# Optimization experiments

Hardware: AMD Instinct MI355X
Metric: run time of the kernel (lower is better)

Reference implementation:

```python
import jax, jax.numpy as jnp
import numpy as np


def setup_inputs() -> dict:
    key = jax.random.key(0)
    ks = jax.random.split(key, 8)
    B, D, S, H, W = 32, 256, 64, 64, 64
    L = H * W
    return {
        "x": jax.random.normal(ks[0], (B, D, L), jnp.float32),
        "H": H,
        "W": W,
        "w_bcdt": jax.random.normal(ks[1], (3 * S, D), jnp.float32) * 0.02,
        "b_bcdt": jnp.zeros((3 * S,), jnp.float32),
        "w_dw": jax.random.normal(ks[2], (3 * S, 1, 3, 3), jnp.float32) * 0.1,
        "b_dw": jnp.zeros((3 * S,), jnp.float32),
        "w_hz": jax.random.normal(ks[3], (2 * D, D), jnp.float32) * 0.02,
        "b_hz": jnp.zeros((2 * D,), jnp.float32),
        "w_out": jax.random.normal(ks[4], (D, D), jnp.float32) * 0.02,
        "b_out": jnp.zeros((D,), jnp.float32),
        "A_param": jax.random.uniform(ks[5], (S,), jnp.float32, minval=1.0, maxval=16.0),
        "D_param": jnp.ones((1,), jnp.float32),
    }


def reference(x, H, W, w_bcdt, b_bcdt, w_dw, b_dw, w_hz, b_hz, w_out, b_out, A_param, D_param):
    batch, d_model, L = x.shape
    S = A_param.shape[0]
    # BCdt_proj: pointwise conv1d -> (B, 3S, L)
    bcdt = jnp.einsum('oc,bcl->bol', w_bcdt, x) + b_bcdt[None, :, None]
    # depthwise 3x3 conv over (H, W)
    x4 = bcdt.reshape(batch, 3 * S, H, W)
    x4 = jax.lax.conv_general_dilated(
        x4, w_dw, window_strides=(1, 1), padding=((1, 1), (1, 1)),
        dimension_numbers=('NCHW', 'OIHW', 'NCHW'), feature_group_count=3 * S,
    ) + b_dw[None, :, None, None]
    bcdt = x4.reshape(batch, 3 * S, L)
    Bm, Cm, dt = jnp.split(bcdt, 3, axis=1)  # each (B, S, L)
    # gating: softmax over sequence dim L
    Aw = jax.nn.softmax(dt + A_param[None, :, None], axis=-1)
    AB = Aw * Bm  # (B, S, L)
    # global state compression: h = x @ AB^T -> (B, d_model, S)
    h = jnp.einsum('bdl,bsl->bds', x, AB)
    # hz_proj (pointwise conv1d over length S)
    hz = jnp.einsum('oc,bcs->bos', w_hz, h) + b_hz[None, :, None]
    h2, z = jnp.split(hz, 2, axis=1)  # each (B, d_inner, S)
    g = h2 * jax.nn.silu(z) + h2 * D_param[0]
    hout = jnp.einsum('oc,bcs->bos', w_out, g) + b_out[None, :, None]  # (B, d_model, S)
    # expand back: y = h @ C -> (B, d_model, L)
    y = jnp.einsum('bds,bsl->bdl', hout, Cm).reshape(batch, d_model, H, W)
    return (y, hout)
```

## Files before the change

kernel.cpp:

```cpp
#include <hip/hip_runtime.h>
#include <math.h>

#define B_  32
#define D_  256
#define L_  4096
#define S_  64
#define C3_ 192

#define YSZ    ((size_t)B_ * D_ * L_)
#define HOUTSZ ((size_t)B_ * D_ * S_)
#define NCHUNK 8

typedef __attribute__((ext_vector_type(8))) short short8;
typedef __attribute__((ext_vector_type(4))) float f32x4;
typedef unsigned short ushort_t;
typedef unsigned int uint_t;

__device__ __forceinline__ short f2bf(float f) {
    __bf16 h = (__bf16)f;
    return __builtin_bit_cast(short, h);
}
__device__ __forceinline__ float bf2f(ushort_t u) {
    return __uint_as_float((uint_t)u << 16);
}
__device__ __forceinline__ short8 ld_cvt8(const float* p) {
    const float4* q = reinterpret_cast<const float4*>(p);
    float4 p0 = q[0], p1 = q[1];
    short8 s;
    s[0] = f2bf(p0.x); s[1] = f2bf(p0.y); s[2] = f2bf(p0.z); s[3] = f2bf(p0.w);
    s[4] = f2bf(p1.x); s[5] = f2bf(p1.y); s[6] = f2bf(p1.z); s[7] = f2bf(p1.w);
    return s;
}

__global__ __launch_bounds__(256) void k1_bcdt_mfma(
    const float* __restrict__ x, const float* __restrict__ w,
    const float* __restrict__ bias, ushort_t* __restrict__ out)
{
    __shared__ __align__(16) short A_lds[192][40];
    __shared__ __align__(16) short B_lds[128][40];
    const int l0 = blockIdx.x * 128;
    const int b  = blockIdx.y;
    const int tid  = threadIdx.x;
    const int lane = tid & 63;
    const int wv   = tid >> 6;
    const int lm   = lane & 15;
    const int kg   = lane >> 4;
    const float* xb = x + (size_t)b * D_ * L_;

    f32x4 acc[12][2];
    #pragma unroll
    for (int mi = 0; mi < 12; ++mi)
        #pragma unroll
        for (int nj = 0; nj < 2; ++nj)
            acc[mi][nj] = (f32x4){0.f, 0.f, 0.f, 0.f};

    for (int k0 = 0; k0 < D_; k0 += 32) {
        if (k0) __syncthreads();
        #pragma unroll
        for (int q = 0; q < 3; ++q) {
            int task = q * 256 + tid;
            int o = task >> 2, kk = (task & 3) * 8;
            *(short8*)&A_lds[o][kk] = ld_cvt8(w + (size_t)o * D_ + k0 + kk);
        }
        {
            int lp = tid & 63;
            int kgs = tid >> 6;
            const float* xp = xb + (size_t)(k0 + kgs * 8) * L_ + l0 + lp * 2;
            float2 v[8];
            #pragma unroll
            for (int r = 0; r < 8; ++r)
                v[r] = *reinterpret_cast<const float2*>(xp + (size_t)r * L_);
            short8 s0, s1;
            #pragma unroll
            for (int r = 0; r < 8; ++r) { s0[r] = f2bf(v[r].x); s1[r] = f2bf(v[r].y); }
            *(short8*)&B_lds[lp * 2][kgs * 8]     = s0;
            *(short8*)&B_lds[lp * 2 + 1][kgs * 8] = s1;
        }
        __syncthreads();
        short8 bb[2];
        #pragma unroll
        for (int nj = 0; nj < 2; ++nj)
            bb[nj] = *(const short8*)&B_lds[wv * 32 + nj * 16 + lm][kg * 8];
        #pragma unroll
        for (int mi = 0; mi < 12; ++mi) {
            short8 a = *(const short8*)&A_lds[mi * 16 + lm][kg * 8];
            #pragma unroll
            for (int nj = 0; nj < 2; ++nj)
                acc[mi][nj] = __builtin_amdgcn_mfma_f32_16x16x32_bf16(
                    a, bb[nj], acc[mi][nj], 0, 0, 0);
        }
    }
    ushort_t* ob = out + (size_t)b * C3_ * L_;
    const int col = l0 + wv * 32 + lm;
    #pragma unroll
    for (int mi = 0; mi < 12; ++mi) {
        #pragma unroll
        for (int r = 0; r < 4; ++r) {
            int o = mi * 16 + kg * 4 + r;
            float bv = bias[o];
            #pragma unroll
            for (int nj = 0; nj < 2; ++nj)
                ob[(size_t)o * L_ + col + nj * 16] =
                    (ushort_t)f2bf(acc[mi][nj][r] + bv);
        }
    }
}

__global__ __launch_bounds__(256) void k2_conv(
    const ushort_t* __restrict__ pre, const float* __restrict__ wdw,
    const float* __restrict__ bdw, ushort_t* __restrict__ cm,
    ushort_t* __restrict__ ab)
{
    __shared__ float sm[66][66];
    __shared__ float red[4];
    const int t   = blockIdx.x;
    const int b   = blockIdx.y;
    const int s   = t & 63;
    const int tid = threadIdx.x;

    for (int i = tid; i < 66 * 66; i += 256) (&sm[0][0])[i] = 0.f;
    __syncthreads();

    if (t < 64) {
        const int c = 64 + s;
        const uint_t* ip32 = reinterpret_cast<const uint_t*>(
            pre + ((size_t)b * C3_ + c) * L_);
        for (int p2 = tid; p2 < 2048; p2 += 256) {
            uint_t v = ip32[p2];
            int q = p2 * 2;
            sm[(q >> 6) + 1][(q & 63) + 1] = bf2f((ushort_t)(v & 0xffffu));
            sm[(q >> 6) + 1][(q & 63) + 2] = bf2f((ushort_t)(v >> 16));
        }
        __syncthreads();
        const float* wp = wdw + c * 9;
        float w00 = wp[0], w01 = wp[1], w02 = wp[2],
              w10 = wp[3], w11 = wp[4], w12 = wp[5],
              w20 = wp[6], w21 = wp[7], w22 = wp[8];
        float bb = bdw[c];
        ushort_t* op = cm + ((size_t)b * S_ + s) * L_;
        for (int p = tid; p < 4096; p += 256) {
            int yy = p >> 6, xx = p & 63;
            float v = bb
                + sm[yy][xx] * w00     + sm[yy][xx + 1] * w01     + sm[yy][xx + 2] * w02
                + sm[yy + 1][xx] * w10 + sm[yy + 1][xx + 1] * w11 + sm[yy + 1][xx + 2] * w12
                + sm[yy + 2][xx] * w20 + sm[yy + 2][xx + 1] * w21 + sm[yy + 2][xx + 2] * w22;
            op[p] = (ushort_t)f2bf(v);
        }
        return;
    }

    const int cd = 128 + s;
    {
        const uint_t* ip32 = reinterpret_cast<const uint_t*>(
            pre + ((size_t)b * C3_ + cd) * L_);
        for (int p2 = tid; p2 < 2048; p2 += 256) {
            uint_t v = ip32[p2];
            int q = p2 * 2;
            sm[(q >> 6) + 1][(q & 63) + 1] = bf2f((ushort_t)(v & 0xffffu));
            sm[(q >> 6) + 1][(q & 63) + 2] = bf2f((ushort_t)(v >> 16));
        }
    }
    __syncthreads();
    float dt[16];
    {
        const float* wp = wdw + cd * 9;
        float w00 = wp[0], w01 = wp[1], w02 = wp[2],
              w10 = wp[3], w11 = wp[4], w12 = wp[5],
              w20 = wp[6], w21 = wp[7], w22 = wp[8];
        float bb = bdw[cd];
        #pragma unroll
        for (int i = 0; i < 16; ++i) {
            int p = tid + 256 * i;
            int yy = p >> 6, xx = p & 63;
            dt[i] = bb
                + sm[yy][xx] * w00     + sm[yy][xx + 1] * w01     + sm[yy][xx + 2] * w02
                + sm[yy + 1][xx] * w10 + sm[yy + 1][xx + 1] * w11 + sm[yy + 1][xx + 2] * w12
                + sm[yy + 2][xx] * w20 + sm[yy + 2][xx + 1] * w21 + sm[yy + 2][xx + 2] * w22;
        }
    }
    float mx = dt[0];
    #pragma unroll
    for (int i = 1; i < 16; ++i) mx = fmaxf(mx, dt[i]);
    #pragma unroll
    for (int off = 32; off >= 1; off >>= 1) mx = fmaxf(mx, __shfl_xor(mx, off, 64));
    if ((tid & 63) == 0) red[tid >> 6] = mx;
    __syncthreads();
    mx = fmaxf(fmaxf(red[0], red[1]), fmaxf(red[2], red[3]));
    float e[16];
    float lsum = 0.f;
    #pragma unroll
    for (int i = 0; i < 16; ++i) { e[i] = expf(dt[i] - mx); lsum += e[i]; }
    #pragma unroll
    for (int off = 32; off >= 1; off >>= 1) lsum += __shfl_xor(lsum, off, 64);
    __syncthreads();
    if ((tid & 63) == 0) red[tid >> 6] = lsum;
    __syncthreads();
    const float inv = 1.f / (red[0] + red[1] + red[2] + red[3]);
    {
        const uint_t* ip32 = reinterpret_cast<const uint_t*>(
            pre + ((size_t)b * C3_ + s) * L_);
        for (int p2 = tid; p2 < 2048; p2 += 256) {
            uint_t v = ip32[p2];
            int q = p2 * 2;
            sm[(q >> 6) + 1][(q & 63) + 1] = bf2f((ushort_t)(v & 0xffffu));
            sm[(q >> 6) + 1][(q & 63) + 2] = bf2f((ushort_t)(v >> 16));
        }
    }
    __syncthreads();
    {
        const float* wp = wdw + s * 9;
        float w00 = wp[0], w01 = wp[1], w02 = wp[2],
              w10 = wp[3], w11 = wp[4], w12 = wp[5],
              w20 = wp[6], w21 = wp[7], w22 = wp[8];
        float bb = bdw[s];
        ushort_t* op = ab + ((size_t)b * S_ + s) * L_;
        #pragma unroll
        for (int i = 0; i < 16; ++i) {
            int p = tid + 256 * i;
            int yy = p >> 6, xx = p & 63;
            float bm = bb
                + sm[yy][xx] * w00     + sm[yy][xx + 1] * w01     + sm[yy][xx + 2] * w02
                + sm[yy + 1][xx] * w10 + sm[yy + 1][xx + 1] * w11 + sm[yy + 1][xx + 2] * w12
                + sm[yy + 2][xx] * w20 + sm[yy + 2][xx + 1] * w21 + sm[yy + 2][xx + 2] * w22;
            op[p] = (ushort_t)f2bf(e[i] * inv * bm);
        }
    }
}

__global__ __launch_bounds__(256) void k3_hpart_mfma(
    const float* __restrict__ x, const ushort_t* __restrict__ ab,
    float* __restrict__ hp)
{
    const int dt    = blockIdx.x;
    const int b     = blockIdx.y;
    const int chunk = blockIdx.z;
    const int tid  = threadIdx.x;
    const int lane = tid & 63;
    const int wv   = tid >> 6;
    const int wr   = wv >> 1, wc = wv & 1;
    const int lm   = lane & 15, kg = lane >> 4;
    const int d_base = dt * 128 + wr * 64;
    const int s_base = wc * 32;
    const float*    xb  = x  + (size_t)b * D_ * L_;
    const ushort_t* abb = ab + (size_t)b * S_ * L_;

    f32x4 acc[4][2];
    #pragma unroll
    for (int mi = 0; mi < 4; ++mi)
        #pragma unroll
        for (int nj = 0; nj < 2; ++nj)
            acc[mi][nj] = (f32x4){0.f, 0.f, 0.f, 0.f};

    #pragma unroll 2
    for (int ks = 0; ks < 16; ++ks) {
        const int l = chunk * 512 + ks * 32 + kg * 8;
        short8 bfr[2];
        #pragma unroll
        for (int nj = 0; nj < 2; ++nj)
            bfr[nj] = *reinterpret_cast<const short8*>(
                abb + (size_t)(s_base + nj * 16 + lm) * L_ + l);
        #pragma unroll
        for (int mi = 0; mi < 4; ++mi) {
            short8 a = ld_cvt8(xb + (size_t)(d_base + mi * 16 + lm) * L_ + l);
            #pragma unroll
            for (int nj = 0; nj < 2; ++nj)
                acc[mi][nj] = __builtin_amdgcn_mfma_f32_16x16x32_bf16(
                    a, bfr[nj], acc[mi][nj], 0, 0, 0);
        }
    }
    float* hpo = hp + (size_t)chunk * HOUTSZ + (size_t)b * D_ * S_;
    #pragma unroll
    for (int mi = 0; mi < 4; ++mi)
        #pragma unroll
        for (int r = 0; r < 4; ++r) {
            int d = d_base + mi * 16 + kg * 4 + r;
            #pragma unroll
            for (int nj = 0; nj < 2; ++nj)
                hpo[(size_t)d * S_ + s_base + nj * 16 + lm] = acc[mi][nj][r];
        }
}

__global__ __launch_bounds__(256) void k4a_gate(
    const float* __restrict__ hp, const float* __restrict__ whz,
    const float* __restrict__ bhz, const float* __restrict__ Dp,
    float* __restrict__ g)
{
    __shared__ float Ah[16][68];
    __shared__ float Az[16][68];
    __shared__ float Bs[16][64];
    const int o0 = blockIdx.x * 64;
    const int b  = blockIdx.y;
    const int tid = threadIdx.x;
    const int tx = tid & 15, ty = tid >> 4;
    float acch[4][4] = {}, accz[4][4] = {};
    const float* hb = hp + (size_t)b * D_ * S_;
    for (int k0 = 0; k0 < D_; k0 += 16) {
        {
            int o = tid & 15, k = tid >> 4;
            #pragma unroll
            for (int i = 0; i < 4; ++i) {
                Ah[k][o + 16 * i] = whz[(size_t)(o0 + o + 16 * i) * D_ + k0 + k];
                Az[k][o + 16 * i] = whz[(size_t)(o0 + o + 16 * i + 256) * D_ + k0 + k];
            }
        }
        {
            int s = tid & 63, k = tid >> 6;
            #pragma unroll
            for (int i = 0; i < 4; ++i) {
                float sum = 0.f;
                #pragma unroll
                for (int c = 0; c < NCHUNK; ++c)
                    sum += hb[(size_t)c * HOUTSZ + (size_t)(k0 + k + 4 * i) * S_ + s];
                Bs[k + 4 * i][s] = sum;
            }
        }
        __syncthreads();
        #pragma unroll
        for (int k = 0; k < 16; ++k) {
            float ah[4], az[4], bb[4];
            #pragma unroll
            for (int i = 0; i < 4; ++i) { ah[i] = Ah[k][ty * 4 + i]; az[i] = Az[k][ty * 4 + i]; }
            #pragma unroll
            for (int j = 0; j < 4; ++j) bb[j] = Bs[k][tx * 4 + j];
            #pragma unroll
            for (int i = 0; i < 4; ++i)
                #pragma unroll
                for (int j = 0; j < 4; ++j) {
                    acch[i][j] += ah[i] * bb[j];
                    accz[i][j] += az[i] * bb[j];
                }
        }
        __syncthreads();
    }
    const float dp = Dp[0];
    #pragma unroll
    for (int i = 0; i < 4; ++i) {
        int o = o0 + ty * 4 + i;
        float bh = bhz[o], bz = bhz[o + 256];
        #pragma unroll
        for (int j = 0; j < 4; ++j) {
            float h2 = acch[i][j] + bh;
            float z  = accz[i][j] + bz;
            float sil = z / (1.f + expf(-z));
            g[((size_t)b * D_ + o) * S_ + tx * 4 + j] = h2 * (sil + dp);
        }
    }
}

__global__ __launch_bounds__(256) void k4b_hout(
    const float* __restrict__ g, const float* __restrict__ wout,
    const float* __restrict__ bout, float* __restrict__ hout)
{
    __shared__ float At[16][68];
    __shared__ float Bs[16][64];
    const int o0 = blockIdx.x * 64;
    const int b  = blockIdx.y;
    const int tid = threadIdx.x;
    const int tx = tid & 15, ty = tid >> 4;
    float acc[4][4] = {};
    const float* gb = g + (size_t)b * D_ * S_;
    for (int k0 = 0; k0 < D_; k0 += 16) {
        {
            int o = tid & 15, k = tid >> 4;
            #pragma unroll
            for (int i = 0; i < 4; ++i)
                At[k][o + 16 * i] = wout[(size_t)(o0 + o + 16 * i) * D_ + k0 + k];
        }
        {
            int s = tid & 63, k = tid >> 6;
            #pragma unroll
            for (int i = 0; i < 4; ++i)
                Bs[k + 4 * i][s] = gb[(size_t)(k0 + k + 4 * i) * S_ + s];
        }
        __syncthreads();
        #pragma unroll
        for (int k = 0; k < 16; ++k) {
            float a[4], bb[4];
            #pragma unroll
            for (int i = 0; i < 4; ++i) a[i] = At[k][ty * 4 + i];
            #pragma unroll
            for (int j = 0; j < 4; ++j) bb[j] = Bs[k][tx * 4 + j];
            #pragma unroll
            for (int i = 0; i < 4; ++i)
                #pragma unroll
                for (int j = 0; j < 4; ++j)
                    acc[i][j] += a[i] * bb[j];
        }
        __syncthreads();
    }
    #pragma unroll
    for (int i = 0; i < 4; ++i) {
        int o = o0 + ty * 4 + i;
        float bv = bout[o];
        #pragma unroll
        for (int j = 0; j < 4; ++j)
            hout[((size_t)b * D_ + o) * S_ + tx * 4 + j] = acc[i][j] + bv;
    }
}

__global__ __launch_bounds__(256) void k5_expand_mfma(
    const float* __restrict__ hout, const ushort_t* __restrict__ cm,
    float* __restrict__ y)
{
    __shared__ __align__(16) short A_lds[64][72];
    __shared__ __align__(16) short B_lds[128][72];
    const int l0 = blockIdx.x * 128;
    const int d0 = blockIdx.y * 64;
    const int b  = blockIdx.z;
    const int tid  = threadIdx.x;
    const int lane = tid & 63;
    const int wv   = tid >> 6;
    const int lm   = lane & 15, kg = lane >> 4;

    #pragma unroll
    for (int q = 0; q < 2; ++q) {
        int task = q * 256 + tid;
        int d = task >> 3, sg = (task & 7) * 8;
        *(short8*)&A_lds[d][sg] = ld_cvt8(hout + ((size_t)b * D_ + d0 + d) * S_ + sg);
    }
    #pragma unroll
    for (int q = 0; q < 4; ++q) {
        int l = tid & 127;
        int sg = (q * 2 + (tid >> 7)) * 8;
        const ushort_t* cp = cm + ((size_t)b * S_ + sg) * L_ + l0 + l;
        short8 s;
        #pragma unroll
        for (int r = 0; r < 8; ++r) s[r] = (short)cp[(size_t)r * L_];
        *(short8*)&B_lds[l][sg] = s;
    }
    __syncthreads();

    f32x4 acc[4][2];
    #pragma unroll
    for (int mi = 0; mi < 4; ++mi)
        #pragma unroll
        for (int nj = 0; nj < 2; ++nj)
            acc[mi][nj] = (f32x4){0.f, 0.f, 0.f, 0.f};
    #pragma unroll
    for (int ks = 0; ks < 2; ++ks) {
        short8 bb[2];
        #pragma unroll
        for (int nj = 0; nj < 2; ++nj)
            bb[nj] = *(const short8*)&B_lds[wv * 32 + nj * 16 + lm][ks * 32 + kg * 8];
        #pragma unroll
        for (int mi = 0; mi < 4; ++mi) {
            short8 a = *(const short8*)&A_lds[mi * 16 + lm][ks * 32 + kg * 8];
            #pragma unroll
            for (int nj = 0; nj < 2; ++nj)
                acc[mi][nj] = __builtin_amdgcn_mfma_f32_16x16x32_bf16(
                    a, bb[nj], acc[mi][nj], 0, 0, 0);
        }
    }
    const int col = l0 + wv * 32 + lm;
    #pragma unroll
    for (int mi = 0; mi < 4; ++mi)
        #pragma unroll
        for (int r = 0; r < 4; ++r)
            #pragma unroll
            for (int nj = 0; nj < 2; ++nj)
                y[((size_t)b * D_ + d0 + mi * 16 + kg * 4 + r) * L_ + col + nj * 16]
                    = acc[mi][nj][r];
}

extern "C" void kernel_launch(void* const* d_in, const int* in_sizes, int n_in,
                              void* d_out, int out_size, void* d_ws, size_t ws_size,
                              hipStream_t stream)
{
    const float* x      = (const float*)d_in[0];
    const float* w_bcdt = (const float*)d_in[3];
    const float* b_bcdt = (const float*)d_in[4];
    const float* w_dw   = (const float*)d_in[5];
    const float* b_dw   = (const float*)d_in[6];
    const float* w_hz   = (const float*)d_in[7];
    const float* b_hz   = (const float*)d_in[8];
    const float* w_out  = (const float*)d_in[9];
    const float* b_out  = (const float*)d_in[10];
    const float* Dp     = (const float*)d_in[12];

    char* base = (char*)d_ws;
    ushort_t* pre_bf = (ushort_t*)(base);
    ushort_t* ab_bf  = (ushort_t*)(base + 50331648);
    ushort_t* cm_bf  = (ushort_t*)(base + 67108864);
    float*    hp     = (float*)   (base + 83886080);
    float*    g      = (float*)   (base + 100663296);

    float* y    = (float*)d_out;
    float* hout = (float*)d_out + YSZ;

    k1_bcdt_mfma  <<<dim3(32, 32),        256, 0, stream>>>(x, w_bcdt, b_bcdt, pre_bf);
    k2_conv       <<<dim3(128, 32),       256, 0, stream>>>(pre_bf, w_dw, b_dw, cm_bf, ab_bf);
    k3_hpart_mfma <<<dim3(2, 32, NCHUNK), 256, 0, stream>>>(x, ab_bf, hp);
    k4a_gate      <<<dim3(4, 32),         256, 0, stream>>>(hp, w_hz, b_hz, Dp, g);
    k4b_hout      <<<dim3(4, 32),         256, 0, stream>>>(g, w_out, b_out, hout);
    k5_expand_mfma<<<dim3(32, 4, 32),     256, 0, stream>>>(hout, cm_bf, y);
}
```

Before: 212.5 us.

## Pre-pack weight fragments, double-buffer x tiles, and emit bf16 x for reuse

Result: slower. 222.6 us (+4.7%).

```diff
diff --git a/kernel.cpp b/kernel.cpp
--- a/kernel.cpp
+++ b/kernel.cpp
@@ -32,12 +32,25 @@
     return s;
 }
 
+__global__ __launch_bounds__(256) void k0_wfrag(
+    const float* __restrict__ w, ushort_t* __restrict__ wfrag)
+{
+    int gid  = blockIdx.x * 256 + threadIdx.x;
+    int lane = gid & 63;
+    int f    = gid >> 6;
+    int step = f / 12, mi = f - step * 12;
+    int o  = mi * 16 + (lane & 15);
+    int kk = step * 32 + (lane >> 4) * 8;
+    short8 s = ld_cvt8(w + (size_t)o * D_ + kk);
+    *(short8*)(wfrag + (size_t)gid * 8) = s;
+}
+
 __global__ __launch_bounds__(256) void k1_bcdt_mfma(
-    const float* __restrict__ x, const float* __restrict__ w,
-    const float* __restrict__ bias, ushort_t* __restrict__ out)
-{
-    __shared__ __align__(16) short A_lds[192][40];
-    __shared__ __align__(16) short B_lds[128][40];
+    const float* __restrict__ x, const ushort_t* __restrict__ wfrag,
+    const float* __restrict__ bias, ushort_t* __restrict__ out,
+    ushort_t* __restrict__ xbf)
+{
+    __shared__ __align__(16) short B_lds[2][128][40];
     const int l0 = blockIdx.x * 128;
     const int b  = blockIdx.y;
     const int tid  = threadIdx.x;
@@ -45,7 +58,10 @@
     const int wv   = tid >> 6;
     const int lm   = lane & 15;
     const int kg   = lane >> 4;
+    const int lp   = tid & 63;
+    const int kgs  = tid >> 6;
     const float* xb = x + (size_t)b * D_ * L_;
+    uint_t* xo = (uint_t*)(xbf + (size_t)b * D_ * L_);
 
     f32x4 acc[12][2];
     #pragma unroll
@@ -54,40 +70,42 @@
         for (int nj = 0; nj < 2; ++nj)
             acc[mi][nj] = (f32x4){0.f, 0.f, 0.f, 0.f};
 
-    for (int k0 = 0; k0 < D_; k0 += 32) {
-        if (k0) __syncthreads();
-        #pragma unroll
-        for (int q = 0; q < 3; ++q) {
-            int task = q * 256 + tid;
-            int o = task >> 2, kk = (task & 3) * 8;
-            *(short8*)&A_lds[o][kk] = ld_cvt8(w + (size_t)o * D_ + k0 + kk);
-        }
-        {
-            int lp = tid & 63;
-            int kgs = tid >> 6;
-            const float* xp = xb + (size_t)(k0 + kgs * 8) * L_ + l0 + lp * 2;
-            float2 v[8];
-            #pragma unroll
-            for (int r = 0; r < 8; ++r)
-                v[r] = *reinterpret_cast<const float2*>(xp + (size_t)r * L_);
-            short8 s0, s1;
-            #pragma unroll
-            for (int r = 0; r < 8; ++r) { s0[r] = f2bf(v[r].x); s1[r] = f2bf(v[r].y); }
-            *(short8*)&B_lds[lp * 2][kgs * 8]     = s0;
-            *(short8*)&B_lds[lp * 2 + 1][kgs * 8] = s1;
-        }
+    auto STAGE = [&](int step, int buf) {
+        const int k0 = step * 32;
+        const float* xp = xb + (size_t)(k0 + kgs * 8) * L_ + l0 + lp * 2;
+        float2 v[8];
+        #pragma unroll
+        for (int r = 0; r < 8; ++r)
+            v[r] = *reinterpret_cast<const float2*>(xp + (size_t)r * L_);
+        short8 s0, s1;
+        #pragma unroll
+        for (int r = 0; r < 8; ++r) { s0[r] = f2bf(v[r].x); s1[r] = f2bf(v[r].y); }
+        *(short8*)&B_lds[buf][lp * 2][kgs * 8]     = s0;
+        *(short8*)&B_lds[buf][lp * 2 + 1][kgs * 8] = s1;
+        #pragma unroll
+        for (int r = 0; r < 8; ++r) {
+            uint_t pk = (uint_t)(ushort_t)s0[r] | ((uint_t)(ushort_t)s1[r] << 16);
+            xo[((size_t)(k0 + kgs * 8 + r) * L_ + l0) / 2 + lp] = pk;
+        }
+    };
+
+    STAGE(0, 0);
+    for (int step = 0; step < 8; ++step) {
         __syncthreads();
-        short8 bb[2];
+        if (step < 7) STAGE(step + 1, (step + 1) & 1);
+        const int cb = step & 1;
+        short8 bbf[2];
         #pragma unroll
         for (int nj = 0; nj < 2; ++nj)
-            bb[nj] = *(const short8*)&B_lds[wv * 32 + nj * 16 + lm][kg * 8];
+            bbf[nj] = *(const short8*)&B_lds[cb][wv * 32 + nj * 16 + lm][kg * 8];
+        const ushort_t* wf = wfrag + ((size_t)step * 12 * 64 + lane) * 8;
         #pragma unroll
         for (int mi = 0; mi < 12; ++mi) {
-            short8 a = *(const short8*)&A_lds[mi * 16 + lm][kg * 8];
+            short8 a = *(const short8*)(wf + (size_t)mi * 64 * 8);
             #pragma unroll
             for (int nj = 0; nj < 2; ++nj)
                 acc[mi][nj] = __builtin_amdgcn_mfma_f32_16x16x32_bf16(
-                    a, bb[nj], acc[mi][nj], 0, 0, 0);
+                    a, bbf[nj], acc[mi][nj], 0, 0, 0);
         }
     }
     ushort_t* ob = out + (size_t)b * C3_ * L_;
@@ -228,7 +246,7 @@
 }
 
 __global__ __launch_bounds__(256) void k3_hpart_mfma(
-    const float* __restrict__ x, const ushort_t* __restrict__ ab,
+    const ushort_t* __restrict__ xbf, const ushort_t* __restrict__ ab,
     float* __restrict__ hp)
 {
     const int dt    = blockIdx.x;
@@ -241,8 +259,8 @@
     const int lm   = lane & 15, kg = lane >> 4;
     const int d_base = dt * 128 + wr * 64;
     const int s_base = wc * 32;
-    const float*    xb  = x  + (size_t)b * D_ * L_;
-    const ushort_t* abb = ab + (size_t)b * S_ * L_;
+    const ushort_t* xbb = xbf + (size_t)b * D_ * L_;
+    const ushort_t* abb = ab  + (size_t)b * S_ * L_;
 
     f32x4 acc[4][2];
     #pragma unroll
@@ -261,7 +279,8 @@
                 abb + (size_t)(s_base + nj * 16 + lm) * L_ + l);
         #pragma unroll
         for (int mi = 0; mi < 4; ++mi) {
-            short8 a = ld_cvt8(xb + (size_t)(d_base + mi * 16 + lm) * L_ + l);
+            short8 a = *reinterpret_cast<const short8*>(
+                xbb + (size_t)(d_base + mi * 16 + lm) * L_ + l);
             #pragma unroll
             for (int nj = 0; nj < 2; ++nj)
                 acc[mi][nj] = __builtin_amdgcn_mfma_f32_16x16x32_bf16(
@@ -479,17 +498,20 @@
 
     char* base = (char*)d_ws;
     ushort_t* pre_bf = (ushort_t*)(base);
-    ushort_t* ab_bf  = (ushort_t*)(base + 50331648);
-    ushort_t* cm_bf  = (ushort_t*)(base + 67108864);
-    float*    hp     = (float*)   (base + 83886080);
-    float*    g      = (float*)   (base + 100663296);
+    ushort_t* xbf    = (ushort_t*)(base + 50331648);
+    ushort_t* ab_bf  = (ushort_t*)(base + 117440512);
+    ushort_t* cm_bf  = (ushort_t*)(base + 134217728);
+    float*    hp     = (float*)   (base);
+    float*    g      = (float*)   (base + 16777216);
+    ushort_t* wfrag  = (ushort_t*)(base + 150994944);
 
     float* y    = (float*)d_out;
     float* hout = (float*)d_out + YSZ;
 
-    k1_bcdt_mfma  <<<dim3(32, 32),        256, 0, stream>>>(x, w_bcdt, b_bcdt, pre_bf);
+    k0_wfrag      <<<24,                  256, 0, stream>>>(w_bcdt, wfrag);
+    k1_bcdt_mfma  <<<dim3(32, 32),        256, 0, stream>>>(x, wfrag, b_bcdt, pre_bf, xbf);
     k2_conv       <<<dim3(128, 32),       256, 0, stream>>>(pre_bf, w_dw, b_dw, cm_bf, ab_bf);
-    k3_hpart_mfma <<<dim3(2, 32, NCHUNK), 256, 0, stream>>>(x, ab_bf, hp);
+    k3_hpart_mfma <<<dim3(2, 32, NCHUNK), 256, 0, stream>>>(xbf, ab_bf, hp);
     k4a_gate      <<<dim3(4, 32),         256, 0, stream>>>(hp, w_hz, b_hz, Dp, g);
     k4b_hout      <<<dim3(4, 32),         256, 0, stream>>>(g, w_out, b_out, hout);
     k5_expand_mfma<<<dim3(32, 4, 32),     256, 0, stream>>>(hout, cm_bf, y);
```
